# Kernel optimization log

Hardware: AMD Instinct MI355X
Metric: run time of the kernel (lower is better)

Reference implementation:

```python
import math
import jax, jax.numpy as jnp
import numpy as np


def setup_inputs() -> dict:
    key = jax.random.key(0)
    k1, k2 = jax.random.split(key)
    N, C, K = 1024, 4096, 16384
    x = jax.random.normal(k1, (N, C), dtype=jnp.float32)
    # xavier_normal for (C, K): std = sqrt(2/(C+K))
    w_std = math.sqrt(2.0 / (C + K))
    weights = jax.random.normal(k2, (C, K), dtype=jnp.float32) * w_std
    std = jnp.float32(10.0)
    return {"x": x, "weights": weights, "std": std}


def reference(x, weights, std):
    # x: (N, C); weights: (C, K)
    N, C = x.shape
    K = weights.shape[1]
    side = int(math.sqrt(K))

    # Squared distances ||w_k - x_n||^2 via expansion (same math as
    # norm(weights[None] - x[..., None], dim=1)**2, without the (N,C,K) tensor)
    x2 = jnp.sum(x * x, axis=1, keepdims=True)            # (N, 1)
    w2 = jnp.sum(weights * weights, axis=0)[None, :]       # (1, K)
    xw = jnp.einsum('nc,ck->nk', x, weights)               # (N, K) GEMM
    norms2 = jnp.maximum(x2 + w2 - 2.0 * xw, 0.0)          # (N, K)

    # Best matching unit (detached in original)
    bmu = jnp.argmin(norms2, axis=-1)                      # (N,) int

    # 2D radial basis over the side x side grid, centered at BMU
    row = (bmu // side).astype(jnp.float32)
    col = (bmu % side).astype(jnp.float32)
    t = jnp.arange(side, dtype=jnp.float32)
    gi, gj = jnp.meshgrid(t, t, indexing='ij')
    grid = jnp.stack([gi.reshape(-1), gj.reshape(-1)], axis=-1)  # (K, 2)
    pt = jnp.stack([row, col], axis=-1)[:, None, :]              # (N, 1, 2)
    d2 = jnp.sum((grid[None] - pt) ** 2, axis=-1)                # (N, K)
    phi = jnp.exp(-0.5 * d2 / (std ** 2))
    phi = phi / jnp.sum(phi, axis=-1, keepdims=True)

    return norms2 * phi
```

## Files before the change

kernel.cpp:

```cpp
#include <hip/hip_runtime.h>
#include <stdint.h>

#define NROWS 1024
#define CDIM  4096
#define KDIM  16384
#define SIDE  128

typedef __attribute__((ext_vector_type(8))) short short8;
typedef __attribute__((ext_vector_type(4))) float f32x4;

static __device__ __forceinline__ unsigned short f2bf(float f) {
  unsigned u = __float_as_uint(f);
  u += 0x7fffu + ((u >> 16) & 1u);
  return (unsigned short)(u >> 16);
}
static __device__ __forceinline__ float bf2f(unsigned short h) {
  return __uint_as_float(((unsigned)h) << 16);
}

#define GLOAD_LDS16(g, l)                                                     \
  __builtin_amdgcn_global_load_lds(                                           \
      (const __attribute__((address_space(1))) void*)(g),                     \
      (__attribute__((address_space(3))) void*)(l), 16, 0, 0)

#define SWZ(o) ((o) ^ (((o) >> 3) & 0x70))

__global__ __launch_bounds__(256) void k_prep(const float* __restrict__ x,
                                              unsigned short* __restrict__ xh,
                                              float* __restrict__ x2,
                                              float* __restrict__ w2) {
  const int n = blockIdx.x, t = threadIdx.x;
  __shared__ float rv[4];
  if (n < 64) w2[n * 256 + t] = 0.f;
  const float* row = x + (size_t)n * CDIM;
  unsigned short* xrow = xh + (size_t)n * CDIM;
  float s = 0.f;
#pragma unroll
  for (int i = 0; i < 4; i++) {
    int e = (t + i * 256) * 4;
    float4 v = *(const float4*)(row + e);
    ushort4 hv;
    hv.x = f2bf(v.x); hv.y = f2bf(v.y); hv.z = f2bf(v.z); hv.w = f2bf(v.w);
    *(ushort4*)(xrow + e) = hv;
    s += v.x * v.x + v.y * v.y + v.z * v.z + v.w * v.w;
  }
#pragma unroll
  for (int off = 32; off > 0; off >>= 1) s += __shfl_down(s, off);
  if ((t & 63) == 0) rv[t >> 6] = s;
  __syncthreads();
  if (t == 0) x2[n] = rv[0] + rv[1] + rv[2] + rv[3];
}

__global__ __launch_bounds__(256) void k_wconv(const float* __restrict__ w,
                                               unsigned short* __restrict__ whT,
                                               unsigned short* __restrict__ wlT,
                                               float* __restrict__ w2) {
  __shared__ float T[64][65];
  const int k0 = blockIdx.x * 64, c0 = blockIdx.y * 64;
  const int t = threadIdx.x;
#pragma unroll
  for (int i = 0; i < 4; i++) {
    int e = i * 1024 + t * 4;
    int cr = e >> 6, kc = e & 63;
    float4 v = *(const float4*)(w + (size_t)(c0 + cr) * KDIM + k0 + kc);
    T[cr][kc] = v.x; T[cr][kc + 1] = v.y; T[cr][kc + 2] = v.z; T[cr][kc + 3] = v.w;
  }
  __syncthreads();
#pragma unroll
  for (int i = 0; i < 4; i++) {
    int e = i * 1024 + t * 4;
    int kr = e >> 6, cc = e & 63;
    ushort4 hv, lv;
    float f0 = T[cc + 0][kr], f1 = T[cc + 1][kr];
    float f2 = T[cc + 2][kr], f3 = T[cc + 3][kr];
    hv.x = f2bf(f0); lv.x = f2bf(f0 - bf2f(hv.x));
    hv.y = f2bf(f1); lv.y = f2bf(f1 - bf2f(hv.y));
    hv.z = f2bf(f2); lv.z = f2bf(f2 - bf2f(hv.z));
    hv.w = f2bf(f3); lv.w = f2bf(f3 - bf2f(hv.w));
    size_t off = (size_t)(k0 + kr) * CDIM + c0 + cc;
    *(ushort4*)(whT + off) = hv;
    *(ushort4*)(wlT + off) = lv;
    float s = f0 * f0 + f1 * f1 + f2 * f2 + f3 * f3;
#pragma unroll
    for (int off2 = 8; off2 > 0; off2 >>= 1) s += __shfl_down(s, off2);
    if ((t & 15) == 0) atomicAdd(&w2[k0 + kr], s);
  }
}

__global__ __launch_bounds__(512, 2) void k_gemm(
    const unsigned short* __restrict__ xh,
    const unsigned short* __restrict__ whT,
    const float* __restrict__ x2, const float* __restrict__ w2,
    float* __restrict__ out) {
  extern __shared__ char smem[];
  const int t = threadIdx.x;
  const int b = blockIdx.x;
  const int L = (b & 7) * 32 + (b >> 3);
  const int m0 = (L & 3) * 256, n0 = (L >> 2) * 256;
  const int lane = t & 63, wid = t >> 6;
  const int wrow = (wid >> 2) * 128;
  const int wcol = (wid & 3) * 64;
  const int rlo = lane & 15;
  const int kgb = (lane >> 4) * 16;

  int rowS[4], cbS[4];
  uint32_t loffS[4];
#pragma unroll
  for (int i = 0; i < 4; i++) {
    int o_lin = (i * 512 + t) * 16;
    int o_log = SWZ(o_lin);
    rowS[i] = o_log >> 7;
    cbS[i] = (o_log & 127) >> 1;
    loffS[i] = i * 8192 + wid * 1024;
  }

  f32x4 acc[8][4];
#pragma unroll
  for (int m = 0; m < 8; m++)
#pragma unroll
    for (int n = 0; n < 4; n++) acc[m][n] = (f32x4){0.f, 0.f, 0.f, 0.f};

#define STAGE_TILE(tt, d)                                                     \
  {                                                                           \
    const int c0s = (tt) * 64;                                                \
    char* const dst = smem + (d) * 65536;                                     \
    _Pragma("unroll")                                                         \
    for (int i = 0; i < 4; i++) {                                             \
      size_t ga = (size_t)(m0 + rowS[i]) * CDIM + c0s + cbS[i];               \
      GLOAD_LDS16(xh + ga, dst + loffS[i]);                                   \
    }                                                                         \
    _Pragma("unroll")                                                         \
    for (int i = 0; i < 4; i++) {                                             \
      size_t gb = (size_t)(n0 + rowS[i]) * CDIM + c0s + cbS[i];               \
      GLOAD_LDS16(whT + gb, dst + 32768 + loffS[i]);                          \
    }                                                                         \
  }

  STAGE_TILE(0, 0);

  for (int tl = 0; tl < 64; ++tl) {
    const int cur = tl & 1;
    if (tl < 63) {
      STAGE_TILE(tl + 1, cur ^ 1);
      asm volatile("s_waitcnt vmcnt(8)" ::: "memory");
    } else {
      asm volatile("s_waitcnt vmcnt(0)" ::: "memory");
    }
    asm volatile("s_barrier" ::: "memory");

    const char* const Ab = smem + cur * 65536;
    const char* const Bb = Ab + 32768;
    short8 b_f[4][2];
#pragma unroll
    for (int n = 0; n < 4; n++)
#pragma unroll
      for (int ks = 0; ks < 2; ks++)
        b_f[n][ks] = *(const short8*)(Bb + SWZ((wcol + n * 16 + rlo) * 128 + ks * 64 + kgb));
    __builtin_amdgcn_s_setprio(1);
#pragma unroll
    for (int m = 0; m < 8; m++) {
      short8 a0 = *(const short8*)(Ab + SWZ((wrow + m * 16 + rlo) * 128 + kgb));
      short8 a1 = *(const short8*)(Ab + SWZ((wrow + m * 16 + rlo) * 128 + 64 + kgb));
#pragma unroll
      for (int n = 0; n < 4; n++) {
        acc[m][n] = __builtin_amdgcn_mfma_f32_16x16x32_bf16(a0, b_f[n][0], acc[m][n], 0, 0, 0);
        acc[m][n] = __builtin_amdgcn_mfma_f32_16x16x32_bf16(a1, b_f[n][1], acc[m][n], 0, 0, 0);
      }
    }
    __builtin_amdgcn_s_setprio(0);
    asm volatile("s_barrier" ::: "memory");
  }
#undef STAGE_TILE

  float w2v[4];
#pragma unroll
  for (int n = 0; n < 4; n++) w2v[n] = w2[n0 + wcol + n * 16 + rlo];
#pragma unroll
  for (int m = 0; m < 8; m++) {
#pragma unroll
    for (int j = 0; j < 4; j++) {
      int row = m0 + wrow + m * 16 + (lane >> 4) * 4 + j;
      float xr = x2[row];
      float* orow = out + (size_t)row * KDIM;
#pragma unroll
      for (int n = 0; n < 4; n++) {
        int col = n0 + wcol + n * 16 + rlo;
        float v = xr + w2v[n] - 2.0f * acc[m][n][j];
        orow[col] = v < 0.f ? 0.f : v;
      }
    }
  }
}

__global__ __launch_bounds__(256) void k_fb(const float* __restrict__ x,
                                            const float* __restrict__ w,
                                            float* __restrict__ out) {
  __shared__ float xs[16][65];
  __shared__ float wsm[16][65];
  const int t = threadIdx.x;
  const int n0 = blockIdx.x * 64, k0 = blockIdx.y * 64;
  const int tx = t & 15, ty = t >> 4;
  float acc[4][4];
#pragma unroll
  for (int a = 0; a < 4; a++)
#pragma unroll
    for (int b = 0; b < 4; b++) acc[a][b] = 0.f;
  for (int c0 = 0; c0 < CDIM; c0 += 16) {
#pragma unroll
    for (int i = 0; i < 4; i++) {
      int e = i * 256 + t;
      int nl = e >> 4, cl = e & 15;
      xs[cl][nl] = x[(size_t)(n0 + nl) * CDIM + c0 + cl];
    }
#pragma unroll
    for (int i = 0; i < 4; i++) {
      int e = i * 256 + t;
      int cl = e >> 6, kl = e & 63;
      wsm[cl][kl] = w[(size_t)(c0 + cl) * KDIM + k0 + kl];
    }
    __syncthreads();
#pragma unroll
    for (int c = 0; c < 16; c++)
#pragma unroll
      for (int a = 0; a < 4; a++) {
        float xa = xs[c][ty * 4 + a];
#pragma unroll
        for (int b = 0; b < 4; b++) {
          float d = wsm[c][tx * 4 + b] - xa;
          acc[a][b] += d * d;
        }
      }
    __syncthreads();
  }
#pragma unroll
  for (int a = 0; a < 4; a++)
#pragma unroll
    for (int b = 0; b < 4; b++)
      out[(size_t)(n0 + ty * 4 + a) * KDIM + k0 + tx * 4 + b] = acc[a][b];
}

__global__ __launch_bounds__(256) void k_row(
    float* __restrict__ out, const float* __restrict__ stdp,
    const float* __restrict__ x, const unsigned short* __restrict__ whT,
    const unsigned short* __restrict__ wlT, const float* __restrict__ w2) {
  const int n = blockIdx.x, t = threadIdx.x;
  __shared__ alignas(16) float er[SIDE];
  __shared__ alignas(16) float ec[SIDE];
  __shared__ float rv[4];
  __shared__ float s_red[4];
  __shared__ int cand[128];
  __shared__ int s_ncand;
  __shared__ int s_bmu;
  __shared__ float s_inv;
  float* row = out + (size_t)n * KDIM;

  float bv = 3.4e38f;
#pragma unroll 4
  for (int i = 0; i < 16; i++) {
    float4 v = *(const float4*)(row + (t + i * 256) * 4);
    bv = fminf(fminf(fminf(bv, v.x), fminf(v.y, v.z)), v.w);
  }
#pragma unroll
  for (int off = 32; off > 0; off >>= 1) bv = fminf(bv, __shfl_down(bv, off));
  if ((t & 63) == 0) rv[t >> 6] = bv;
  if (t == 0) s_ncand = 0;
  __syncthreads();
  const float thr = fminf(fminf(rv[0], rv[1]), fminf(rv[2], rv[3])) + 0.05f;

#pragma unroll 4
  for (int i = 0; i < 16; i++) {
    int k = (t + i * 256) * 4;
    float4 v = *(const float4*)(row + k);
    if (v.x <= thr) { int j = atomicAdd(&s_ncand, 1); if (j < 128) cand[j] = k; }
    if (v.y <= thr) { int j = atomicAdd(&s_ncand, 1); if (j < 128) cand[j] = k + 1; }
    if (v.z <= thr) { int j = atomicAdd(&s_ncand, 1); if (j < 128) cand[j] = k + 2; }
    if (v.w <= thr) { int j = atomicAdd(&s_ncand, 1); if (j < 128) cand[j] = k + 3; }
  }
  __syncthreads();
  int nc = s_ncand < 128 ? s_ncand : 128;

  float best = 3.4e38f;
  int bestk = 0x7fffffff;
  const float* xr = x + (size_t)n * CDIM;
  for (int j = 0; j < nc; j++) {
    const int k = cand[j];
    const unsigned short* wh = whT + (size_t)k * CDIM;
    const unsigned short* wl = wlT + (size_t)k * CDIM;
    float s = 0.f;
#pragma unroll
    for (int ii = 0; ii < 2; ii++) {
      int c = (ii * 256 + t) * 8;
      short8 h8 = *(const short8*)(wh + c);
      short8 l8 = *(const short8*)(wl + c);
      float4 xa = *(const float4*)(xr + c);
      float4 xb = *(const float4*)(xr + c + 4);
      s += xa.x * (bf2f((unsigned short)h8[0]) + bf2f((unsigned short)l8[0]));
      s += xa.y * (bf2f((unsigned short)h8[1]) + bf2f((unsigned short)l8[1]));
      s += xa.z * (bf2f((unsigned short)h8[2]) + bf2f((unsigned short)l8[2]));
      s += xa.w * (bf2f((unsigned short)h8[3]) + bf2f((unsigned short)l8[3]));
      s += xb.x * (bf2f((unsigned short)h8[4]) + bf2f((unsigned short)l8[4]));
      s += xb.y * (bf2f((unsigned short)h8[5]) + bf2f((unsigned short)l8[5]));
      s += xb.z * (bf2f((unsigned short)h8[6]) + bf2f((unsigned short)l8[6]));
      s += xb.w * (bf2f((unsigned short)h8[7]) + bf2f((unsigned short)l8[7]));
    }
#pragma unroll
    for (int off = 32; off > 0; off >>= 1) s += __shfl_down(s, off);
    if ((t & 63) == 0) s_red[t >> 6] = s;
    __syncthreads();
    if (t == 0) {
      float dot = s_red[0] + s_red[1] + s_red[2] + s_red[3];
      float sc = w2[k] - 2.0f * dot;
      if (sc < best || (sc == best && k < bestk)) { best = sc; bestk = k; }
    }
    __syncthreads();
  }
  if (t == 0) s_bmu = bestk;
  __syncthreads();

  const int bmu = s_bmu;
  const float sd = stdp[0];
  const float inv2s2 = -0.5f / (sd * sd);
  const float rr = (float)(bmu >> 7), ccol = (float)(bmu & 127);
  if (t < 128) {
    float d = (float)t - rr;
    er[t] = expf(d * d * inv2s2);
  } else {
    int j = t - 128;
    float d = (float)j - ccol;
    ec[j] = expf(d * d * inv2s2);
  }
  __syncthreads();
  if (t == 0) {
    float Sr = 0.f, Sc = 0.f;
    for (int i = 0; i < SIDE; i++) { Sr += er[i]; Sc += ec[i]; }
    s_inv = 1.0f / (Sr * Sc);
  }
  __syncthreads();
  const float inv = s_inv;
#pragma unroll 4
  for (int i = 0; i < 16; i++) {
    int k = (t + i * 256) * 4;
    float4 v = *(const float4*)(row + k);
    float e_r = er[k >> 7] * inv;
    const float4 e4 = *(const float4*)(&ec[k & 127]);
    v.x *= e_r * e4.x;
    v.y *= e_r * e4.y;
    v.z *= e_r * e4.z;
    v.w *= e_r * e4.w;
    *(float4*)(row + k) = v;
  }
}

__global__ __launch_bounds__(256) void k_row_fb(float* __restrict__ out,
                                                const float* __restrict__ stdp) {
  const int n = blockIdx.x, t = threadIdx.x;
  __shared__ alignas(16) float er[SIDE];
  __shared__ alignas(16) float ec[SIDE];
  __shared__ float rv[4];
  __shared__ int ri[4];
  __shared__ float s_inv;
  __shared__ int s_bmu;
  float* row = out + (size_t)n * KDIM;

  float bv = 3.4e38f;
  int bi = 0;
#pragma unroll 4
  for (int i = 0; i < 16; i++) {
    int k = (t + i * 256) * 4;
    float4 v = *(const float4*)(row + k);
    if (v.x < bv) { bv = v.x; bi = k; }
    if (v.y < bv) { bv = v.y; bi = k + 1; }
    if (v.z < bv) { bv = v.z; bi = k + 2; }
    if (v.w < bv) { bv = v.w; bi = k + 3; }
  }
#pragma unroll
  for (int off = 32; off > 0; off >>= 1) {
    float ov = __shfl_down(bv, off);
    int oi = __shfl_down(bi, off);
    if (ov < bv || (ov == bv && oi < bi)) { bv = ov; bi = oi; }
  }
  if ((t & 63) == 0) { rv[t >> 6] = bv; ri[t >> 6] = bi; }
  __syncthreads();
  if (t == 0) {
    for (int i = 1; i < 4; i++)
      if (rv[i] < bv || (rv[i] == bv && ri[i] < bi)) { bv = rv[i]; bi = ri[i]; }
    s_bmu = bi;
  }
  __syncthreads();
  const int bmu = s_bmu;
  const float sd = stdp[0];
  const float inv2s2 = -0.5f / (sd * sd);
  const float rr = (float)(bmu >> 7), ccol = (float)(bmu & 127);
  if (t < 128) {
    float d = (float)t - rr;
    er[t] = expf(d * d * inv2s2);
  } else {
    int j = t - 128;
    float d = (float)j - ccol;
    ec[j] = expf(d * d * inv2s2);
  }
  __syncthreads();
  if (t == 0) {
    float Sr = 0.f, Sc = 0.f;
    for (int i = 0; i < SIDE; i++) { Sr += er[i]; Sc += ec[i]; }
    s_inv = 1.0f / (Sr * Sc);
  }
  __syncthreads();
  const float inv = s_inv;
#pragma unroll 4
  for (int i = 0; i < 16; i++) {
    int k = (t + i * 256) * 4;
    float4 v = *(const float4*)(row + k);
    float e_r = er[k >> 7] * inv;
    const float4 e4 = *(const float4*)(&ec[k & 127]);
    v.x *= e_r * e4.x;
    v.y *= e_r * e4.y;
    v.z *= e_r * e4.z;
    v.w *= e_r * e4.w;
    *(float4*)(row + k) = v;
  }
}

extern "C" void kernel_launch(void* const* d_in, const int* in_sizes, int n_in,
                              void* d_out, int out_size, void* d_ws, size_t ws_size,
                              hipStream_t stream) {
  (void)in_sizes; (void)n_in; (void)out_size;
  const float* x = (const float*)d_in[0];
  const float* w = (const float*)d_in[1];
  const float* stdp = (const float*)d_in[2];
  float* out = (float*)d_out;

  const size_t sz_wT = (size_t)KDIM * CDIM * sizeof(unsigned short);
  const size_t sz_x  = (size_t)NROWS * CDIM * sizeof(unsigned short);
  const size_t need = 2 * sz_wT + sz_x + (size_t)NROWS * 4 + (size_t)KDIM * 4;

  if (ws_size >= need) {
    char* p = (char*)d_ws;
    unsigned short* whT = (unsigned short*)p; p += sz_wT;
    unsigned short* wlT = (unsigned short*)p; p += sz_wT;
    unsigned short* xh  = (unsigned short*)p; p += sz_x;
    float* x2 = (float*)p; p += (size_t)NROWS * 4;
    float* w2 = (float*)p;

    static int lds_ok = -1;
    if (lds_ok < 0)
      lds_ok = (int)hipFuncSetAttribute((const void*)k_gemm,
                                        hipFuncAttributeMaxDynamicSharedMemorySize,
                                        131072);

    k_prep<<<NROWS, 256, 0, stream>>>(x, xh, x2, w2);
    k_wconv<<<dim3(KDIM / 64, CDIM / 64), 256, 0, stream>>>(w, whT, wlT, w2);
    k_gemm<<<256, 512, 131072, stream>>>(xh, whT, x2, w2, out);
    k_row<<<NROWS, 256, 0, stream>>>(out, stdp, x, whT, wlT, w2);
  } else {
    k_fb<<<dim3(NROWS / 64, KDIM / 64), 256, 0, stream>>>(x, w, out);
    k_row_fb<<<NROWS, 256, 0, stream>>>(out, stdp);
  }
}
```

Measured before the change: 303.0 us.

## Triple-buffer B tiles in GEMM and keep row values in registers

```diff
diff --git a/kernel.cpp b/kernel.cpp
--- a/kernel.cpp
+++ b/kernel.cpp
@@ -120,36 +120,43 @@
 #pragma unroll
     for (int n = 0; n < 4; n++) acc[m][n] = (f32x4){0.f, 0.f, 0.f, 0.f};
 
-#define STAGE_TILE(tt, d)                                                     \
+#define STAGE_A(tt)                                                           \
   {                                                                           \
-    const int c0s = (tt) * 64;                                                \
-    char* const dst = smem + (d) * 65536;                                     \
+    const int tc_ = (tt) < 63 ? (tt) : 63;                                    \
+    const int c0s = tc_ * 64;                                                 \
+    char* const dst = smem + (((tt) & 1) * 32768);                            \
     _Pragma("unroll")                                                         \
     for (int i = 0; i < 4; i++) {                                             \
       size_t ga = (size_t)(m0 + rowS[i]) * CDIM + c0s + cbS[i];               \
       GLOAD_LDS16(xh + ga, dst + loffS[i]);                                   \
     }                                                                         \
+  }
+#define STAGE_B(tt)                                                           \
+  {                                                                           \
+    const int tc_ = (tt) < 63 ? (tt) : 63;                                    \
+    const int c0s = tc_ * 64;                                                 \
+    char* const dst = smem + 65536 + (((tt) % 3) * 32768);                    \
     _Pragma("unroll")                                                         \
     for (int i = 0; i < 4; i++) {                                             \
       size_t gb = (size_t)(n0 + rowS[i]) * CDIM + c0s + cbS[i];               \
-      GLOAD_LDS16(whT + gb, dst + 32768 + loffS[i]);                          \
+      GLOAD_LDS16(whT + gb, dst + 32768 + loffS[i] - 32768);                  \
     }                                                                         \
   }
 
-  STAGE_TILE(0, 0);
+  STAGE_A(0);
+  STAGE_B(0);
+  STAGE_B(1);
+  asm volatile("s_waitcnt vmcnt(4)" ::: "memory");
+  asm volatile("s_barrier" ::: "memory");
 
   for (int tl = 0; tl < 64; ++tl) {
-    const int cur = tl & 1;
-    if (tl < 63) {
-      STAGE_TILE(tl + 1, cur ^ 1);
-      asm volatile("s_waitcnt vmcnt(8)" ::: "memory");
-    } else {
-      asm volatile("s_waitcnt vmcnt(0)" ::: "memory");
-    }
+    STAGE_A(tl + 1);
+    STAGE_B(tl + 2);
+    asm volatile("s_waitcnt vmcnt(12)" ::: "memory");
     asm volatile("s_barrier" ::: "memory");
 
-    const char* const Ab = smem + cur * 65536;
-    const char* const Bb = Ab + 32768;
+    const char* const Ab = smem + (tl & 1) * 32768;
+    const char* const Bb = smem + 65536 + (tl % 3) * 32768;
     short8 b_f[4][2];
 #pragma unroll
     for (int n = 0; n < 4; n++)
@@ -170,7 +177,9 @@
     __builtin_amdgcn_s_setprio(0);
     asm volatile("s_barrier" ::: "memory");
   }
-#undef STAGE_TILE
+#undef STAGE_A
+#undef STAGE_B
+  asm volatile("s_waitcnt vmcnt(0)" ::: "memory");
 
   float w2v[4];
 #pragma unroll
@@ -254,11 +263,12 @@
   __shared__ float s_inv;
   float* row = out + (size_t)n * KDIM;
 
+  float4 vals[16];
   float bv = 3.4e38f;
-#pragma unroll 4
+#pragma unroll
   for (int i = 0; i < 16; i++) {
-    float4 v = *(const float4*)(row + (t + i * 256) * 4);
-    bv = fminf(fminf(fminf(bv, v.x), fminf(v.y, v.z)), v.w);
+    vals[i] = *(const float4*)(row + (t + i * 256) * 4);
+    bv = fminf(fminf(fminf(bv, vals[i].x), fminf(vals[i].y, vals[i].z)), vals[i].w);
   }
 #pragma unroll
   for (int off = 32; off > 0; off >>= 1) bv = fminf(bv, __shfl_down(bv, off));
@@ -267,14 +277,13 @@
   __syncthreads();
   const float thr = fminf(fminf(rv[0], rv[1]), fminf(rv[2], rv[3])) + 0.05f;
 
-#pragma unroll 4
+#pragma unroll
   for (int i = 0; i < 16; i++) {
     int k = (t + i * 256) * 4;
-    float4 v = *(const float4*)(row + k);
-    if (v.x <= thr) { int j = atomicAdd(&s_ncand, 1); if (j < 128) cand[j] = k; }
-    if (v.y <= thr) { int j = atomicAdd(&s_ncand, 1); if (j < 128) cand[j] = k + 1; }
-    if (v.z <= thr) { int j = atomicAdd(&s_ncand, 1); if (j < 128) cand[j] = k + 2; }
-    if (v.w <= thr) { int j = atomicAdd(&s_ncand, 1); if (j < 128) cand[j] = k + 3; }
+    if (vals[i].x <= thr) { int j = atomicAdd(&s_ncand, 1); if (j < 128) cand[j] = k; }
+    if (vals[i].y <= thr) { int j = atomicAdd(&s_ncand, 1); if (j < 128) cand[j] = k + 1; }
+    if (vals[i].z <= thr) { int j = atomicAdd(&s_ncand, 1); if (j < 128) cand[j] = k + 2; }
+    if (vals[i].w <= thr) { int j = atomicAdd(&s_ncand, 1); if (j < 128) cand[j] = k + 3; }
   }
   __syncthreads();
   int nc = s_ncand < 128 ? s_ncand : 128;
@@ -337,10 +346,10 @@
   }
   __syncthreads();
   const float inv = s_inv;
-#pragma unroll 4
+#pragma unroll
   for (int i = 0; i < 16; i++) {
     int k = (t + i * 256) * 4;
-    float4 v = *(const float4*)(row + k);
+    float4 v = vals[i];
     float e_r = er[k >> 7] * inv;
     const float4 e4 = *(const float4*)(&ec[k & 127]);
     v.x *= e_r * e4.x;
@@ -446,11 +455,11 @@
     if (lds_ok < 0)
       lds_ok = (int)hipFuncSetAttribute((const void*)k_gemm,
                                         hipFuncAttributeMaxDynamicSharedMemorySize,
-                                        131072);
+                                        163840);
 
     k_prep<<<NROWS, 256, 0, stream>>>(x, xh, x2, w2);
     k_wconv<<<dim3(KDIM / 64, CDIM / 64), 256, 0, stream>>>(w, whT, wlT, w2);
-    k_gemm<<<256, 512, 131072, stream>>>(xh, whT, x2, w2, out);
+    k_gemm<<<256, 512, 163840, stream>>>(xh, whT, x2, w2, out);
     k_row<<<NROWS, 256, 0, stream>>>(out, stdp, x, whT, wlT, w2);
   } else {
     k_fb<<<dim3(NROWS / 64, KDIM / 64), 256, 0, stream>>>(x, w, out);
```

Result: faster. 290.3 us (-4.2%).
